# Kernel tuning notes

Measured on AMD Instinct MI355X. Metric: run time of the kernel, lower is better.

## Reference

```python
import jax, jax.numpy as jnp
import numpy as np

B, N_IN, N_MID, N_OUT = 1048576, 64, 32, 16


def setup_inputs() -> dict:
    key = jax.random.key(0)
    kx, k1, k2 = jax.random.split(key, 3)
    x = jax.random.normal(kx, (B, N_IN), dtype=jnp.float32)
    # Synapse.init_weight uses uniform(-sqrt(1/fan_in), sqrt(1/fan_in)); biases init to 0.0.
    v1 = float(np.sqrt(1.0 / N_IN))
    v2 = float(np.sqrt(1.0 / N_MID))
    W1 = jax.random.uniform(k1, (N_IN, N_MID), dtype=jnp.float32, minval=-v1, maxval=v1)
    W2 = jax.random.uniform(k2, (N_MID, N_OUT), dtype=jnp.float32, minval=-v2, maxval=v2)
    b1 = jnp.zeros((N_MID,), dtype=jnp.float32)
    b2 = jnp.zeros((N_OUT,), dtype=jnp.float32)
    return {"x": x, "W1": W1, "b1": b1, "W2": W2, "b2": b2}


def reference(x, W1, b1, W2, b2):
    # Middle RegularNeurons: sum of k*source_output over dendrites + b, then ReLU.
    h = jax.nn.relu(x @ W1 + b1)          # [B, N_MID]
    # Output DestinationNeurons: sum of dendrites + b, activation=None.
    y = h @ W2 + b2                        # [B, N_OUT]
    return y
```

## Files before the change

kernel.cpp:

```cpp
#include <hip/hip_runtime.h>


#define N_IN  64
#define N_MID 32
#define N_OUT 16

__global__ __launch_bounds__(256) void livenet_mlp_kernel(
    const float* __restrict__ x,
    const float* __restrict__ W1,
    const float* __restrict__ b1,
    const float* __restrict__ W2,
    const float* __restrict__ b2,
    float* __restrict__ y,
    int nrows)
{
    const int row = blockIdx.x * blockDim.x + threadIdx.x;
    if (row >= nrows) return;

    const float4* __restrict__ xr =
        reinterpret_cast<const float4*>(x + (size_t)row * N_IN);
    float4 xv[16];
#pragma unroll
    for (int i = 0; i < 16; ++i) xv[i] = xr[i];

    float h[N_MID];
#pragma unroll
    for (int j = 0; j < N_MID; ++j) h[j] = b1[j];

#pragma unroll
    for (int kk = 0; kk < 16; ++kk) {
        const float xs0 = xv[kk].x;
        const float xs1 = xv[kk].y;
        const float xs2 = xv[kk].z;
        const float xs3 = xv[kk].w;
        const int k = kk * 4;
#pragma unroll
        for (int j = 0; j < N_MID; ++j)
            h[j] = __builtin_fmaf(xs0, W1[(k + 0) * N_MID + j], h[j]);
#pragma unroll
        for (int j = 0; j < N_MID; ++j)
            h[j] = __builtin_fmaf(xs1, W1[(k + 1) * N_MID + j], h[j]);
#pragma unroll
        for (int j = 0; j < N_MID; ++j)
            h[j] = __builtin_fmaf(xs2, W1[(k + 2) * N_MID + j], h[j]);
#pragma unroll
        for (int j = 0; j < N_MID; ++j)
            h[j] = __builtin_fmaf(xs3, W1[(k + 3) * N_MID + j], h[j]);
    }

#pragma unroll
    for (int j = 0; j < N_MID; ++j) h[j] = fmaxf(h[j], 0.0f);

    float yv[N_OUT];
#pragma unroll
    for (int o = 0; o < N_OUT; ++o) yv[o] = b2[o];
#pragma unroll
    for (int j = 0; j < N_MID; ++j) {
        const float hj = h[j];
#pragma unroll
        for (int o = 0; o < N_OUT; ++o)
            yv[o] = __builtin_fmaf(hj, W2[j * N_OUT + o], yv[o]);
    }

    float4* __restrict__ yr = reinterpret_cast<float4*>(y + (size_t)row * N_OUT);
#pragma unroll
    for (int i = 0; i < 4; ++i)
        yr[i] = make_float4(yv[4 * i + 0], yv[4 * i + 1], yv[4 * i + 2], yv[4 * i + 3]);
}

extern "C" void kernel_launch(void* const* d_in, const int* in_sizes, int n_in,
                              void* d_out, int out_size, void* d_ws, size_t ws_size,
                              hipStream_t stream) {
    const float* x  = (const float*)d_in[0];
    const float* W1 = (const float*)d_in[1];
    const float* b1 = (const float*)d_in[2];
    const float* W2 = (const float*)d_in[3];
    const float* b2 = (const float*)d_in[4];
    float* y = (float*)d_out;

    const int nrows = in_sizes[0] / N_IN;
    const int block = 256;
    const int grid = (nrows + block - 1) / block;
    livenet_mlp_kernel<<<grid, block, 0, stream>>>(x, W1, b1, W2, b2, y, nrows);
}
```

Measured before the change: 410.1 us.

## Stage input rows through swizzled LDS for coalesced global loads

Each wave now loads its 64 input rows with fully coalesced float4 reads, where consecutive lanes touch consecutive 16-byte chunks. It transposes them through an XOR-swizzled per-wave shared-memory tile in two halves so each lane recovers its own row. This replaces the old pattern of strided 256-byte-per-lane row loads with poor coalescing. Launch bounds now request 4 blocks per SM for occupancy. The bounds check is removed, so row counts that are not multiples of 256 are silently dropped.

```diff
diff --git a/kernel.cpp b/kernel.cpp
--- a/kernel.cpp
+++ b/kernel.cpp
@@ -4,48 +4,94 @@
 #define N_IN  64
 #define N_MID 32
 #define N_OUT 16
+#define BLOCK 256
 
-__global__ __launch_bounds__(256) void livenet_mlp_kernel(
+__global__ __launch_bounds__(BLOCK, 4) void livenet_mlp_kernel(
     const float* __restrict__ x,
     const float* __restrict__ W1,
     const float* __restrict__ b1,
     const float* __restrict__ W2,
     const float* __restrict__ b2,
-    float* __restrict__ y,
-    int nrows)
+    float* __restrict__ y)
 {
-    const int row = blockIdx.x * blockDim.x + threadIdx.x;
-    if (row >= nrows) return;
+    __shared__ float4 tile[4][512];
 
-    const float4* __restrict__ xr =
-        reinterpret_cast<const float4*>(x + (size_t)row * N_IN);
-    float4 xv[16];
+    const int lane = threadIdx.x & 63;
+    const int wave = threadIdx.x >> 6;
+    const int rowbase = blockIdx.x * BLOCK + wave * 64;
+
+    const float4* __restrict__ xg = reinterpret_cast<const float4*>(x);
+
+    float4 v0[8], v1[8];
 #pragma unroll
-    for (int i = 0; i < 16; ++i) xv[i] = xr[i];
+    for (int i = 0; i < 8; ++i) {
+        const int f  = i * 64 + lane;
+        const int r  = f >> 3;
+        const int c4 = f & 7;
+        const size_t g = (size_t)(rowbase + r) * 16 + c4;
+        v0[i] = xg[g];
+        v1[i] = xg[g + 8];
+    }
 
     float h[N_MID];
 #pragma unroll
     for (int j = 0; j < N_MID; ++j) h[j] = b1[j];
 
 #pragma unroll
-    for (int kk = 0; kk < 16; ++kk) {
-        const float xs0 = xv[kk].x;
-        const float xs1 = xv[kk].y;
-        const float xs2 = xv[kk].z;
-        const float xs3 = xv[kk].w;
-        const int k = kk * 4;
+    for (int i = 0; i < 8; ++i) {
+        const int f  = i * 64 + lane;
+        const int r  = f >> 3;
+        const int c4 = f & 7;
+        tile[wave][r * 8 + (c4 ^ (r & 7))] = v0[i];
+    }
+    asm volatile("s_waitcnt lgkmcnt(0)" ::: "memory");
+    __builtin_amdgcn_wave_barrier();
+
+#pragma unroll
+    for (int c4 = 0; c4 < 8; ++c4) {
+        const float4 xv = tile[wave][lane * 8 + (c4 ^ (lane & 7))];
+        const int k = c4 * 4;
 #pragma unroll
         for (int j = 0; j < N_MID; ++j)
-            h[j] = __builtin_fmaf(xs0, W1[(k + 0) * N_MID + j], h[j]);
+            h[j] = __builtin_fmaf(xv.x, W1[(k + 0) * N_MID + j], h[j]);
 #pragma unroll
         for (int j = 0; j < N_MID; ++j)
-            h[j] = __builtin_fmaf(xs1, W1[(k + 1) * N_MID + j], h[j]);
+            h[j] = __builtin_fmaf(xv.y, W1[(k + 1) * N_MID + j], h[j]);
 #pragma unroll
         for (int j = 0; j < N_MID; ++j)
-            h[j] = __builtin_fmaf(xs2, W1[(k + 2) * N_MID + j], h[j]);
+            h[j] = __builtin_fmaf(xv.z, W1[(k + 2) * N_MID + j], h[j]);
 #pragma unroll
         for (int j = 0; j < N_MID; ++j)
-            h[j] = __builtin_fmaf(xs3, W1[(k + 3) * N_MID + j], h[j]);
+            h[j] = __builtin_fmaf(xv.w, W1[(k + 3) * N_MID + j], h[j]);
+    }
+    __builtin_amdgcn_wave_barrier();
+
+#pragma unroll
+    for (int i = 0; i < 8; ++i) {
+        const int f  = i * 64 + lane;
+        const int r  = f >> 3;
+        const int c4 = f & 7;
+        tile[wave][r * 8 + (c4 ^ (r & 7))] = v1[i];
+    }
+    asm volatile("s_waitcnt lgkmcnt(0)" ::: "memory");
+    __builtin_amdgcn_wave_barrier();
+
+#pragma unroll
+    for (int c4 = 0; c4 < 8; ++c4) {
+        const float4 xv = tile[wave][lane * 8 + (c4 ^ (lane & 7))];
+        const int k = 32 + c4 * 4;
+#pragma unroll
+        for (int j = 0; j < N_MID; ++j)
+            h[j] = __builtin_fmaf(xv.x, W1[(k + 0) * N_MID + j], h[j]);
+#pragma unroll
+        for (int j = 0; j < N_MID; ++j)
+            h[j] = __builtin_fmaf(xv.y, W1[(k + 1) * N_MID + j], h[j]);
+#pragma unroll
+        for (int j = 0; j < N_MID; ++j)
+            h[j] = __builtin_fmaf(xv.z, W1[(k + 2) * N_MID + j], h[j]);
+#pragma unroll
+        for (int j = 0; j < N_MID; ++j)
+            h[j] = __builtin_fmaf(xv.w, W1[(k + 3) * N_MID + j], h[j]);
     }
 
 #pragma unroll
@@ -62,10 +108,11 @@
             yv[o] = __builtin_fmaf(hj, W2[j * N_OUT + o], yv[o]);
     }
 
-    float4* __restrict__ yr = reinterpret_cast<float4*>(y + (size_t)row * N_OUT);
+    float4* __restrict__ yg =
+        reinterpret_cast<float4*>(y + (size_t)(rowbase + lane) * N_OUT);
 #pragma unroll
     for (int i = 0; i < 4; ++i)
-        yr[i] = make_float4(yv[4 * i + 0], yv[4 * i + 1], yv[4 * i + 2], yv[4 * i + 3]);
+        yg[i] = make_float4(yv[4 * i + 0], yv[4 * i + 1], yv[4 * i + 2], yv[4 * i + 3]);
 }
 
 extern "C" void kernel_launch(void* const* d_in, const int* in_sizes, int n_in,
@@ -76,10 +123,9 @@
     const float* b1 = (const float*)d_in[2];
     const float* W2 = (const float*)d_in[3];
     const float* b2 = (const float*)d_in[4];
-    float* y = (float*)d_out;
+    float* yp = (float*)d_out;
 
     const int nrows = in_sizes[0] / N_IN;
-    const int block = 256;
-    const int grid = (nrows + block - 1) / block;
-    livenet_mlp_kernel<<<grid, block, 0, stream>>>(x, W1, b1, W2, b2, y, nrows);
+    const int grid = nrows / BLOCK;
+    livenet_mlp_kernel<<<grid, BLOCK, 0, stream>>>(x, W1, b1, W2, b2, yp);
 }
```

Result: no change. 412.9 us (+0.7%).

## Compute MLP with split-bf16 MFMA tiles, wave-per-tile loop and LDS transpose

Applied to the files above, without the earlier changes.

Replaces the per-thread scalar FMA MLP with MFMA 16x16x32 bf16 instructions. Each fp32 value is split into high and low bf16 parts and three MFMAs are used to recover near-fp32 accuracy. Each wave processes 8 tiles of 16 rows, prefetching the next x tile into registers and moving the hidden activations through LDS to re-layout them for the second matmul. The goal is to remove the ALU-bound scalar FMA work so the kernel becomes bandwidth-bound. In exchange, the grid assumes the row count divides evenly by 512 and adds some precision risk from the split bf16.

```diff
diff --git a/kernel.cpp b/kernel.cpp
--- a/kernel.cpp
+++ b/kernel.cpp
@@ -1,71 +1,143 @@
 #include <hip/hip_runtime.h>
 
 
-#define N_IN  64
-#define N_MID 32
-#define N_OUT 16
+#define BLOCK 256
+#define TPW   8
+#define LSTR  33
 
-__global__ __launch_bounds__(256) void livenet_mlp_kernel(
+typedef __attribute__((ext_vector_type(8))) short bf16x8;
+typedef __attribute__((ext_vector_type(4))) float f32x4;
+
+static __device__ __forceinline__ short f2bf(float f) {
+    unsigned u = __float_as_uint(f);
+    u += 0x7FFFu + ((u >> 16) & 1u);
+    return (short)(u >> 16);
+}
+static __device__ __forceinline__ float bf2f(short s) {
+    return __uint_as_float(((unsigned)(unsigned short)s) << 16);
+}
+
+__global__ __launch_bounds__(BLOCK, 3) void livenet_mlp_mfma(
     const float* __restrict__ x,
     const float* __restrict__ W1,
     const float* __restrict__ b1,
     const float* __restrict__ W2,
     const float* __restrict__ b2,
-    float* __restrict__ y,
-    int nrows)
+    float* __restrict__ y)
 {
-    const int row = blockIdx.x * blockDim.x + threadIdx.x;
-    if (row >= nrows) return;
+    __shared__ float hlds[4][16 * LSTR];
 
-    const float4* __restrict__ xr =
-        reinterpret_cast<const float4*>(x + (size_t)row * N_IN);
-    float4 xv[16];
+    const int lane = threadIdx.x & 63;
+    const int wave = threadIdx.x >> 6;
+    const int l15  = lane & 15;
+    const int q    = lane >> 4;
+
+    bf16x8 w1h[2][2], w1l[2][2];
 #pragma unroll
-    for (int i = 0; i < 16; ++i) xv[i] = xr[i];
+    for (int s = 0; s < 2; ++s)
+#pragma unroll
+        for (int t = 0; t < 2; ++t)
+#pragma unroll
+            for (int j = 0; j < 8; ++j) {
+                float w = W1[(32 * s + q * 8 + j) * 32 + 16 * t + l15];
+                short hh = f2bf(w);
+                w1h[s][t][j] = hh;
+                w1l[s][t][j] = f2bf(w - bf2f(hh));
+            }
+    bf16x8 w2h, w2l;
+#pragma unroll
+    for (int j = 0; j < 8; ++j) {
+        float w = W2[(q * 8 + j) * 16 + l15];
+        short hh = f2bf(w);
+        w2h[j] = hh;
+        w2l[j] = f2bf(w - bf2f(hh));
+    }
+    float b1v[8];
+#pragma unroll
+    for (int j = 0; j < 8; ++j) b1v[j] = b1[q * 8 + j];
+    const float b2v = b2[l15];
 
-    float h[N_MID];
+    const long tile0 = ((long)blockIdx.x * 4 + wave) * TPW;
+    const float* xb = x + (size_t)tile0 * 1024 + (size_t)l15 * 64 + q * 8;
+    float* hw = &hlds[wave][0];
+
+    f32x4 c0 = *(const f32x4*)(xb + 0);
+    f32x4 c1 = *(const f32x4*)(xb + 4);
+    f32x4 c2 = *(const f32x4*)(xb + 32);
+    f32x4 c3 = *(const f32x4*)(xb + 36);
+
+    for (int t = 0; t < TPW; ++t) {
+        const int tn = (t + 1 < TPW) ? (t + 1) : t;
+        const float* xn = xb + (size_t)tn * 1024;
+        f32x4 n0 = *(const f32x4*)(xn + 0);
+        f32x4 n1 = *(const f32x4*)(xn + 4);
+        f32x4 n2 = *(const f32x4*)(xn + 32);
+        f32x4 n3 = *(const f32x4*)(xn + 36);
+
+        float xs[16];
 #pragma unroll
-    for (int j = 0; j < N_MID; ++j) h[j] = b1[j];
+        for (int j = 0; j < 4; ++j) {
+            xs[j]      = c0[j];
+            xs[4 + j]  = c1[j];
+            xs[8 + j]  = c2[j];
+            xs[12 + j] = c3[j];
+        }
+        bf16x8 ah[2], al[2];
+#pragma unroll
+        for (int s = 0; s < 2; ++s)
+#pragma unroll
+            for (int j = 0; j < 8; ++j) {
+                float v = xs[s * 8 + j];
+                short hh = f2bf(v);
+                ah[s][j] = hh;
+                al[s][j] = f2bf(v - bf2f(hh));
+            }
+
+        f32x4 acc0 = {0.f, 0.f, 0.f, 0.f};
+        f32x4 acc1 = {0.f, 0.f, 0.f, 0.f};
+#pragma unroll
+        for (int s = 0; s < 2; ++s) {
+            acc0 = __builtin_amdgcn_mfma_f32_16x16x32_bf16(ah[s], w1h[s][0], acc0, 0, 0, 0);
+            acc0 = __builtin_amdgcn_mfma_f32_16x16x32_bf16(al[s], w1h[s][0], acc0, 0, 0, 0);
+            acc0 = __builtin_amdgcn_mfma_f32_16x16x32_bf16(ah[s], w1l[s][0], acc0, 0, 0, 0);
+            acc1 = __builtin_amdgcn_mfma_f32_16x16x32_bf16(ah[s], w1h[s][1], acc1, 0, 0, 0);
+            acc1 = __builtin_amdgcn_mfma_f32_16x16x32_bf16(al[s], w1h[s][1], acc1, 0, 0, 0);
+            acc1 = __builtin_amdgcn_mfma_f32_16x16x32_bf16(ah[s], w1l[s][1], acc1, 0, 0, 0);
+        }
 
 #pragma unroll
-    for (int kk = 0; kk < 16; ++kk) {
-        const float xs0 = xv[kk].x;
-        const float xs1 = xv[kk].y;
-        const float xs2 = xv[kk].z;
-        const float xs3 = xv[kk].w;
-        const int k = kk * 4;
+        for (int r = 0; r < 4; ++r) {
+            hw[(q * 4 + r) * LSTR + l15]      = acc0[r];
+            hw[(q * 4 + r) * LSTR + 16 + l15] = acc1[r];
+        }
+        asm volatile("s_waitcnt lgkmcnt(0)" ::: "memory");
+        __builtin_amdgcn_wave_barrier();
+
+        float hv[8];
 #pragma unroll
-        for (int j = 0; j < N_MID; ++j)
-            h[j] = __builtin_fmaf(xs0, W1[(k + 0) * N_MID + j], h[j]);
+        for (int j = 0; j < 8; ++j) hv[j] = hw[l15 * LSTR + q * 8 + j];
+
+        bf16x8 fh, fl;
 #pragma unroll
-        for (int j = 0; j < N_MID; ++j)
-            h[j] = __builtin_fmaf(xs1, W1[(k + 1) * N_MID + j], h[j]);
+        for (int j = 0; j < 8; ++j) {
+            float v = fmaxf(hv[j] + b1v[j], 0.0f);
+            short hh = f2bf(v);
+            fh[j] = hh;
+            fl[j] = f2bf(v - bf2f(hh));
+        }
+        __builtin_amdgcn_wave_barrier();
+
+        f32x4 acc2 = {0.f, 0.f, 0.f, 0.f};
+        acc2 = __builtin_amdgcn_mfma_f32_16x16x32_bf16(fh, w2h, acc2, 0, 0, 0);
+        acc2 = __builtin_amdgcn_mfma_f32_16x16x32_bf16(fl, w2h, acc2, 0, 0, 0);
+        acc2 = __builtin_amdgcn_mfma_f32_16x16x32_bf16(fh, w2l, acc2, 0, 0, 0);
+
+        float* yr = y + (size_t)(tile0 + t) * 256 + q * 64 + l15;
 #pragma unroll
-        for (int j = 0; j < N_MID; ++j)
-            h[j] = __builtin_fmaf(xs2, W1[(k + 2) * N_MID + j], h[j]);
-#pragma unroll
-        for (int j = 0; j < N_MID; ++j)
-            h[j] = __builtin_fmaf(xs3, W1[(k + 3) * N_MID + j], h[j]);
+        for (int r = 0; r < 4; ++r) yr[r * 16] = acc2[r] + b2v;
+
+        c0 = n0; c1 = n1; c2 = n2; c3 = n3;
     }
-
-#pragma unroll
-    for (int j = 0; j < N_MID; ++j) h[j] = fmaxf(h[j], 0.0f);
-
-    float yv[N_OUT];
-#pragma unroll
-    for (int o = 0; o < N_OUT; ++o) yv[o] = b2[o];
-#pragma unroll
-    for (int j = 0; j < N_MID; ++j) {
-        const float hj = h[j];
-#pragma unroll
-        for (int o = 0; o < N_OUT; ++o)
-            yv[o] = __builtin_fmaf(hj, W2[j * N_OUT + o], yv[o]);
-    }
-
-    float4* __restrict__ yr = reinterpret_cast<float4*>(y + (size_t)row * N_OUT);
-#pragma unroll
-    for (int i = 0; i < 4; ++i)
-        yr[i] = make_float4(yv[4 * i + 0], yv[4 * i + 1], yv[4 * i + 2], yv[4 * i + 3]);
 }
 
 extern "C" void kernel_launch(void* const* d_in, const int* in_sizes, int n_in,
@@ -76,10 +148,10 @@
     const float* b1 = (const float*)d_in[2];
     const float* W2 = (const float*)d_in[3];
     const float* b2 = (const float*)d_in[4];
-    float* y = (float*)d_out;
+    float* yp = (float*)d_out;
 
-    const int nrows = in_sizes[0] / N_IN;
-    const int block = 256;
-    const int grid = (nrows + block - 1) / block;
-    livenet_mlp_kernel<<<grid, block, 0, stream>>>(x, W1, b1, W2, b2, y, nrows);
+    const int nrows = in_sizes[0] / 64;
+    const int rows_per_block = 4 * TPW * 16;
+    const int grid = nrows / rows_per_block;
+    livenet_mlp_mfma<<<grid, BLOCK, 0, stream>>>(x, W1, b1, W2, b2, yp);
 }
```

New measurement: 378.8 us. 7.6% less time.
